# Kernel optimization log

Measured on AMD Instinct MI355X. Metric: run time of the kernel, lower is better.

## Reference

```python
import jax, jax.numpy as jnp
import numpy as np
import math

B_SZ = 2
SEQ = 4000
D_MODEL = 768
D_INNER = 1536
D_STATE = 16
D_CONV = 4
DT_RANK = 48
NSLICES = 5


def setup_inputs() -> dict:
    key = jax.random.key(0)
    ks = jax.random.split(key, 9)
    s = 0.02
    hidden_states = jax.random.normal(ks[0], (B_SZ, SEQ, D_MODEL), jnp.float32)
    in_proj_w = jax.random.normal(ks[1], (2 * D_INNER, D_MODEL), jnp.float32) * s
    conv_w = jax.random.normal(ks[2], (3, D_INNER, 1, D_CONV), jnp.float32) * 0.3
    x_proj_w = jax.random.normal(ks[3], (3, DT_RANK + 2 * D_STATE, D_INNER), jnp.float32) * s
    dt_proj_w = jax.random.uniform(ks[4], (3, D_INNER, DT_RANK), jnp.float32,
                                   -(DT_RANK ** -0.5), DT_RANK ** -0.5)
    # dt bias: inverse-softplus of dt ~ LogUniform(1e-3, 0.1), as in the torch init
    dt = jnp.exp(jax.random.uniform(ks[5], (3, D_INNER), jnp.float32)
                 * (math.log(0.1) - math.log(1e-3)) + math.log(1e-3))
    dt = jnp.clip(dt, 1e-4, None)
    dt_bias = dt + jnp.log(-jnp.expm1(-dt))
    A = jnp.broadcast_to(jnp.arange(1, D_STATE + 1, dtype=jnp.float32), (D_INNER, D_STATE))
    A_log = jnp.broadcast_to(jnp.log(A), (3, D_INNER, D_STATE))
    D_param = jnp.ones((3, D_INNER), jnp.float32)
    out_proj_w = jax.random.normal(ks[6], (D_MODEL, D_INNER), jnp.float32) * s
    return dict(hidden_states=hidden_states, in_proj_w=in_proj_w, conv_w=conv_w,
                x_proj_w=x_proj_w, dt_proj_w=dt_proj_w, dt_bias=dt_bias,
                A_log=A_log, D_param=D_param, out_proj_w=out_proj_w)


def _mamba_branch(xz, cw, xpw, dpw, db, A_log, Dv):
    # xz: [B, 2*d_inner, L]. Equivalent of mamba_inner_fn_no_out_proj.
    x, z = jnp.split(xz, 2, axis=1)                      # [B, d, L] each
    # depthwise causal conv1d (left pad d_conv-1, output length L)
    xc = jax.lax.conv_general_dilated(
        x, cw, window_strides=(1,), padding=[(D_CONV - 1, 0)],
        feature_group_count=D_INNER,
        dimension_numbers=('NCH', 'OIH', 'NCH'))
    x = jax.nn.silu(xc)
    x_dbl = jnp.einsum('bdl,ed->bel', x, xpw)            # [B, dt_rank+2n, L]
    dtr, Bm, Cm = jnp.split(x_dbl, [DT_RANK, DT_RANK + D_STATE], axis=1)
    delta = jax.nn.softplus(jnp.einsum('brl,dr->bdl', dtr, dpw) + db[None, :, None])
    A = -jnp.exp(A_log)                                  # [d, n]

    def step(h, inp):
        d_t, x_t, B_t, C_t = inp                         # [B,d],[B,d],[B,n],[B,n]
        h = h * jnp.exp(d_t[..., None] * A) + (d_t * x_t)[..., None] * B_t[:, None, :]
        y = jnp.einsum('bdn,bn->bd', h, C_t)
        return h, y

    inputs = (jnp.moveaxis(delta, 2, 0), jnp.moveaxis(x, 2, 0),
              jnp.moveaxis(Bm, 2, 0), jnp.moveaxis(Cm, 2, 0))
    h0 = jnp.zeros((x.shape[0], D_INNER, D_STATE), x.dtype)
    _, ys = jax.lax.scan(step, h0, inputs)               # ys: [L, B, d]
    y = jnp.moveaxis(ys, 0, 2)                           # [B, d, L]
    y = y + Dv[None, :, None] * x
    return y * jax.nn.silu(z)


def reference(hidden_states, in_proj_w, conv_w, x_proj_w, dt_proj_w, dt_bias,
              A_log, D_param, out_proj_w):
    b, l, _ = hidden_states.shape
    lc = l // NSLICES
    xz = jnp.einsum('bld,ed->bel', hidden_states, in_proj_w)   # [B, 2d, L]
    # branch 0: forward
    out0 = _mamba_branch(xz, conv_w[0], x_proj_w[0], dt_proj_w[0], dt_bias[0],
                         A_log[0], D_param[0])
    # branch 1: reversed sequence
    out1 = _mamba_branch(xz[:, :, ::-1], conv_w[1], x_proj_w[1], dt_proj_w[1],
                         dt_bias[1], A_log[1], D_param[1])[:, :, ::-1]
    # branch 2: slice-interleaved (chunk into nslices, stack, flatten)
    xz2 = xz.reshape(b, 2 * D_INNER, NSLICES, lc).transpose(0, 1, 3, 2).reshape(b, 2 * D_INNER, l)
    out2 = _mamba_branch(xz2, conv_w[2], x_proj_w[2], dt_proj_w[2], dt_bias[2],
                         A_log[2], D_param[2])
    out2 = out2.reshape(b, D_INNER, lc, NSLICES).transpose(0, 1, 3, 2).reshape(b, D_INNER, l)
    out = out0 + out1 + out2
    return jnp.einsum('bdl,od->blo', out, out_proj_w)          # [B, L, d_model]
```

## Files before the change

kernel.cpp:

```cpp
#include <hip/hip_runtime.h>
#include <math.h>

#define L_SEQ 4000
#define DM 768
#define DI 1536
#define DS 16
#define DTRK 48
#define NCH 50
#define LC 80
#define NBL 8000

typedef __attribute__((ext_vector_type(8))) short short8;
typedef __attribute__((ext_vector_type(8))) unsigned short ushort8;
typedef __attribute__((ext_vector_type(4))) unsigned short ushort4v;
typedef __attribute__((ext_vector_type(4))) float floatx4;
typedef __attribute__((ext_vector_type(2))) float float2v;

__device__ __forceinline__ float silu_f(float x) { return x / (1.f + __expf(-x)); }
__device__ __forceinline__ float softplus_f(float x) {
  return fmaxf(x, 0.f) + __logf(1.f + __expf(-fabsf(x)));
}
__device__ __forceinline__ int map_t(int branch, int t) {
  if (branch == 0) return t;
  if (branch == 1) return L_SEQ - 1 - t;
  return (t % 5) * 800 + t / 5;
}
__device__ __forceinline__ unsigned short f2bf(float f) {
  unsigned int u = __float_as_uint(f);
  u = (u + 0x7fffu + ((u >> 16) & 1u)) >> 16;
  return (unsigned short)u;
}
__device__ __forceinline__ float bf2f(unsigned short u) {
  return __uint_as_float(((unsigned int)u) << 16);
}
__device__ __forceinline__ void glds16(const void* g, void* l) {
  __builtin_amdgcn_global_load_lds((const __attribute__((address_space(1))) void*)g,
                                   (__attribute__((address_space(3))) void*)l, 16, 0, 0);
}
__device__ __forceinline__ void pow_ladder2(float E1, float2v* dc2) {
  float E2 = E1 * E1;
  float E4 = E2 * E2;
  float E8 = E4 * E4;
  float2v v4 = {E4, E4}, v8 = {E8, E8};
  dc2[0] = (float2v){E1, E2};
  dc2[1] = dc2[0] * (float2v){E2, E2};
  dc2[2] = dc2[0] * v4;
  dc2[3] = dc2[1] * v4;
  dc2[4] = dc2[0] * v8;
  dc2[5] = dc2[1] * v8;
  dc2[6] = dc2[2] * v8;
  dc2[7] = dc2[3] * v8;
}

__device__ __forceinline__ void cast_seg(const float* __restrict__ src,
                                         unsigned short* __restrict__ dst,
                                         int blk, int n) {
  int i = (blk * 256 + (int)threadIdx.x) * 8;
  if (i >= n) return;
  float4 v0 = *(const float4*)&src[i];
  float4 v1 = *(const float4*)&src[i + 4];
  ushort8 r;
  r[0] = f2bf(v0.x); r[1] = f2bf(v0.y); r[2] = f2bf(v0.z); r[3] = f2bf(v0.w);
  r[4] = f2bf(v1.x); r[5] = f2bf(v1.y); r[6] = f2bf(v1.z); r[7] = f2bf(v1.w);
  *(ushort8*)&dst[i] = r;
}
__global__ __launch_bounds__(256) void k_cast5(const float* s0, unsigned short* d0,
                                               const float* s1, unsigned short* d1,
                                               const float* s2, unsigned short* d2,
                                               const float* s3, unsigned short* d3,
                                               const float* s4, unsigned short* d4) {
  int blk = blockIdx.x;
  if (blk < 3000)      cast_seg(s0, d0, blk,        6144000);
  else if (blk < 4152) cast_seg(s1, d1, blk - 3000, 2359296);
  else if (blk < 4728) cast_seg(s2, d2, blk - 4152, 1179648);
  else if (blk < 4836) cast_seg(s3, d3, blk - 4728, 221184);
  else                 cast_seg(s4, d4, blk - 4836, 368640);
}

template <int KDIM, int KA, int MODE, int MT, int NBLK, int BMAJ = 0, int NTW = 128>
__global__ __launch_bounds__(256) void k_gemm_bt(const unsigned short* __restrict__ A,
                                                 const unsigned short* __restrict__ B,
                                                 float* __restrict__ O0f,
                                                 unsigned short* __restrict__ O0h,
                                                 unsigned short* __restrict__ O1h) {
  __shared__ unsigned short As[128 * 32];
  __shared__ unsigned short Bs[NTW * 32];
  constexpr int Q = NBLK / 8, R = NBLK % 8;
  constexpr int NFR = NTW / 32;
  int xcd = blockIdx.x & 7;
  int slot = blockIdx.x >> 3;
  int start = xcd * Q + (xcd < R ? xcd : R);
  int j = start + slot;
  int m0 = (j % MT) * 128;
  int n0 = (j / MT) * NTW;
  int tid = threadIdx.x;
  int lane = tid & 63;
  int wm = (tid >> 6) & 1;
  int wn = tid >> 7;
  int srow = tid >> 2;
  int skof = (((tid & 3) ^ ((tid >> 3) & 3)) * 8);
  int brow0 = n0 + srow;       if (brow0 >= NBL) brow0 = NBL - 1;
  int brow1 = n0 + srow + 64;  if (brow1 >= NBL) brow1 = NBL - 1;
  size_t rb0a = 0, rb0b = 0, rb0c = 0, rb1a = 0, rb1b = 0, rb1c = 0;
  if (BMAJ) {
    int bb0 = brow0 >= L_SEQ ? 1 : 0, l0 = brow0 - bb0 * L_SEQ;
    int t1_0 = L_SEQ - 1 - l0;
    int t2_0 = 5 * (l0 % 800) + l0 / 800;
    rb0a = ((size_t)(0 + bb0) * L_SEQ + l0) * DI;
    rb0b = ((size_t)(2 + bb0) * L_SEQ + t1_0) * DI;
    rb0c = ((size_t)(4 + bb0) * L_SEQ + t2_0) * DI;
    if (NTW == 128) {
      int bb1 = brow1 >= L_SEQ ? 1 : 0, l1 = brow1 - bb1 * L_SEQ;
      int t1_1 = L_SEQ - 1 - l1;
      int t2_1 = 5 * (l1 % 800) + l1 / 800;
      rb1a = ((size_t)(0 + bb1) * L_SEQ + l1) * DI;
      rb1b = ((size_t)(2 + bb1) * L_SEQ + t1_1) * DI;
      rb1c = ((size_t)(4 + bb1) * L_SEQ + t2_1) * DI;
    }
  }
  floatx4 zero = {0.f, 0.f, 0.f, 0.f};
  floatx4 acc[4][NFR];
#pragma unroll
  for (int i = 0; i < 4; ++i)
#pragma unroll
    for (int j2 = 0; j2 < NFR; ++j2) acc[i][j2] = zero;
  int ar = wm * 64 + (lane & 15);
  int br = wn * (NTW / 2) + (lane & 15);
  int kq = (((lane >> 4) ^ ((lane >> 1) & 3)) * 8);
  int brnk = 0, dd0 = 0;
  for (int k0 = 0; k0 < KDIM; k0 += 32) {
    int ka = (k0 % KA);
    glds16(&A[(size_t)(m0 + srow) * KA + ka + skof],      &As[tid * 8]);
    glds16(&A[(size_t)(m0 + srow + 64) * KA + ka + skof], &As[tid * 8 + 2048]);
    if (BMAJ) {
      size_t b0 = brnk == 0 ? rb0a : (brnk == 1 ? rb0b : rb0c);
      glds16(&B[b0 + dd0 + skof], &Bs[tid * 8]);
      if (NTW == 128) {
        size_t b1 = brnk == 0 ? rb1a : (brnk == 1 ? rb1b : rb1c);
        glds16(&B[b1 + dd0 + skof], &Bs[tid * 8 + 2048]);
      }
      dd0 += 32;
      if (dd0 == DI) { dd0 = 0; ++brnk; }
    } else {
      glds16(&B[(size_t)brow0 * KDIM + k0 + skof], &Bs[tid * 8]);
      if (NTW == 128)
        glds16(&B[(size_t)brow1 * KDIM + k0 + skof], &Bs[tid * 8 + 2048]);
    }
    __syncthreads();
    short8 a[4], b[NFR];
#pragma unroll
    for (int i = 0; i < 4; ++i) a[i] = *(const short8*)&As[(ar + i * 16) * 32 + kq];
#pragma unroll
    for (int i = 0; i < NFR; ++i) b[i] = *(const short8*)&Bs[(br + i * 16) * 32 + kq];
#pragma unroll
    for (int mt = 0; mt < 4; ++mt)
#pragma unroll
      for (int nt = 0; nt < NFR; ++nt)
        acc[mt][nt] = __builtin_amdgcn_mfma_f32_16x16x32_bf16(a[mt], b[nt], acc[mt][nt], 0, 0, 0);
    __syncthreads();
  }
  int mq = m0 + wm * 64 + ((lane >> 4) << 2);
  int nq = n0 + wn * (NTW / 2) + (lane & 15);
#pragma unroll
  for (int nt = 0; nt < NFR; ++nt) {
    int n = nq + nt * 16;
    if (n >= NBL) continue;
#pragma unroll
    for (int mt = 0; mt < 4; ++mt) {
      int m = mq + mt * 16;
      floatx4 v = acc[mt][nt];
      if (MODE == 0) {
        *(floatx4*)&O0f[(size_t)n * DM + m] = v;
      } else {
        if (m < DI) {
          ushort4v r;
          r[0] = f2bf(v[0]); r[1] = f2bf(v[1]); r[2] = f2bf(v[2]); r[3] = f2bf(v[3]);
          *(ushort4v*)&O0h[(size_t)n * DI + m] = r;
        } else {
          ushort4v r;
          r[0] = f2bf(silu_f(v[0])); r[1] = f2bf(silu_f(v[1]));
          r[2] = f2bf(silu_f(v[2])); r[3] = f2bf(silu_f(v[3]));
          *(ushort4v*)&O1h[(size_t)n * DI + m - DI] = r;
        }
      }
    }
  }
}

__global__ __launch_bounds__(256) void k_conv_all(const unsigned short* __restrict__ xTB,
                                                  const float* __restrict__ cw_all,
                                                  unsigned short* __restrict__ xaB) {
  int z = blockIdx.z;
  int brn = z >> 1, b = z & 1;
  int d = blockIdx.x * 256 + threadIdx.x;
  int t0 = blockIdx.y * 8;
  const unsigned short* xrow = xTB + (size_t)b * L_SEQ * DI;
  float4 w = *(const float4*)&cw_all[((size_t)brn * DI + d) * 4];
  float xm3 = (t0 >= 3) ? bf2f(xrow[(size_t)map_t(brn, t0 - 3) * DI + d]) : 0.f;
  float xm2 = (t0 >= 2) ? bf2f(xrow[(size_t)map_t(brn, t0 - 2) * DI + d]) : 0.f;
  float xm1 = (t0 >= 1) ? bf2f(xrow[(size_t)map_t(brn, t0 - 1) * DI + d]) : 0.f;
#pragma unroll
  for (int i = 0; i < 8; ++i) {
    int t = t0 + i;
    float xc = bf2f(xrow[(size_t)map_t(brn, t) * DI + d]);
    float xa = silu_f(fmaf(w.w, xc, fmaf(w.z, xm1, fmaf(w.y, xm2, w.x * xm3))));
    xaB[((size_t)z * L_SEQ + t) * DI + d] = f2bf(xa);
    xm3 = xm2; xm2 = xm1; xm1 = xc;
  }
}

__global__ __launch_bounds__(256) void k_xprojm(const unsigned short* __restrict__ xpwB,
                                                const unsigned short* __restrict__ xaB,
                                                unsigned short* __restrict__ dtrB,
                                                float* __restrict__ BC) {
  __shared__ unsigned short As[128 * 32];
  __shared__ unsigned short Bs[128 * 32];
  int z = blockIdx.z;
  int brn = z >> 1;
  int n0 = blockIdx.x * 128;
  int tid = threadIdx.x;
  int lane = tid & 63;
  int wm = (tid >> 6) & 1;
  int wn = tid >> 7;
  int srow = tid >> 2;
  int skof = (((tid & 3) ^ ((tid >> 3) & 3)) * 8);
  int arow0 = srow;       if (arow0 > 79) arow0 = 79;
  int arow1 = srow + 64;  if (arow1 > 79) arow1 = 79;
  int brow0 = n0 + srow;       if (brow0 >= L_SEQ) brow0 = L_SEQ - 1;
  int brow1 = n0 + srow + 64;  if (brow1 >= L_SEQ) brow1 = L_SEQ - 1;
  const unsigned short* A = xpwB + (size_t)brn * 80 * DI;
  const unsigned short* Bm = xaB + (size_t)z * L_SEQ * DI;
  floatx4 zero = {0.f, 0.f, 0.f, 0.f};
  floatx4 acc[4][4];
#pragma unroll
  for (int i = 0; i < 4; ++i)
#pragma unroll
    for (int j = 0; j < 4; ++j) acc[i][j] = zero;
  int ar = wm * 64 + (lane & 15);
  int br = wn * 64 + (lane & 15);
  int kq = (((lane >> 4) ^ ((lane >> 1) & 3)) * 8);
  for (int k0 = 0; k0 < DI; k0 += 32) {
    glds16(&A[(size_t)arow0 * DI + k0 + skof], &As[tid * 8]);
    glds16(&A[(size_t)arow1 * DI + k0 + skof], &As[tid * 8 + 2048]);
    glds16(&Bm[(size_t)brow0 * DI + k0 + skof], &Bs[tid * 8]);
    glds16(&Bm[(size_t)brow1 * DI + k0 + skof], &Bs[tid * 8 + 2048]);
    __syncthreads();
    short8 a[4], b[4];
#pragma unroll
    for (int i = 0; i < 4; ++i) a[i] = *(const short8*)&As[(ar + i * 16) * 32 + kq];
#pragma unroll
    for (int i = 0; i < 4; ++i) b[i] = *(const short8*)&Bs[(br + i * 16) * 32 + kq];
#pragma unroll
    for (int mt = 0; mt < 4; ++mt)
#pragma unroll
      for (int nt = 0; nt < 4; ++nt)
        acc[mt][nt] = __builtin_amdgcn_mfma_f32_16x16x32_bf16(a[mt], b[nt], acc[mt][nt], 0, 0, 0);
    __syncthreads();
  }
  int mq = wm * 64 + ((lane >> 4) << 2);
  int nq = n0 + wn * 64 + (lane & 15);
#pragma unroll
  for (int nt = 0; nt < 4; ++nt) {
    int t = nq + nt * 16;
    if (t >= L_SEQ) continue;
#pragma unroll
    for (int mt = 0; mt < 4; ++mt) {
      int j = mq + mt * 16;
      if (j >= 80) continue;
      floatx4 v = acc[mt][nt];
      if (j < 48) {
        ushort4v r;
        r[0] = f2bf(v[0]); r[1] = f2bf(v[1]); r[2] = f2bf(v[2]); r[3] = f2bf(v[3]);
        *(ushort4v*)&dtrB[((size_t)z * L_SEQ + t) * DTRK + j] = r;
      } else {
#pragma unroll
        for (int r = 0; r < 4; ++r)
          BC[((size_t)z * 32 + (j + r - 48)) * L_SEQ + t] = v[r];
      }
    }
  }
}

__global__ __launch_bounds__(256) void k_dtg(const unsigned short* __restrict__ dpwB,
                                             const unsigned short* __restrict__ dtrB,
                                             const float* __restrict__ dbias,
                                             unsigned short* __restrict__ dT) {
  __shared__ unsigned short As[128 * 64];
  __shared__ unsigned short Bs[128 * 64];
  int z = blockIdx.z;
  int brn = z >> 1;
  int m0 = blockIdx.y * 128;
  int n0 = blockIdx.x * 128;
  int tid = threadIdx.x;
  int lane = tid & 63;
  int wm = (tid >> 6) & 1;
  int wn = tid >> 7;
  {
    int zr = tid >> 1, zs = 6 + (tid & 1);
    ushort8 zz = {0, 0, 0, 0, 0, 0, 0, 0};
    *(ushort8*)&As[zr * 64 + ((zs ^ (zr & 7)) << 3)] = zz;
    *(ushort8*)&Bs[zr * 64 + ((zs ^ (zr & 7)) << 3)] = zz;
  }
  {
    int row = tid >> 1;
    int p0 = (tid & 1) * 3;
    const unsigned short* Ag = dpwB + (size_t)brn * DI * DTRK + (size_t)(m0 + row) * DTRK;
    int bro = n0 + row; if (bro > L_SEQ - 1) bro = L_SEQ - 1;
    const unsigned short* Bg = dtrB + ((size_t)z * L_SEQ + bro) * DTRK;
#pragma unroll
    for (int i = 0; i < 3; ++i) {
      int slot = p0 + i;
      int off = (slot ^ (row & 7)) << 3;
      *(ushort8*)&As[row * 64 + off] = *(const ushort8*)&Ag[slot << 3];
      *(ushort8*)&Bs[row * 64 + off] = *(const ushort8*)&Bg[slot << 3];
    }
  }
  __syncthreads();
  int ar = wm * 64 + (lane & 15);
  int brr = wn * 64 + (lane & 15);
  int kslot = lane >> 4;
  floatx4 zero = {0.f, 0.f, 0.f, 0.f};
  floatx4 acc[4][4];
#pragma unroll
  for (int i = 0; i < 4; ++i)
#pragma unroll
    for (int j = 0; j < 4; ++j) acc[i][j] = zero;
#pragma unroll
  for (int kk = 0; kk < 2; ++kk) {
    short8 a[4], b[4];
    int slot = kk * 4 + kslot;
#pragma unroll
    for (int i = 0; i < 4; ++i) {
      int r = ar + i * 16;
      a[i] = *(const short8*)&As[r * 64 + ((slot ^ (r & 7)) << 3)];
    }
#pragma unroll
    for (int i = 0; i < 4; ++i) {
      int r = brr + i * 16;
      b[i] = *(const short8*)&Bs[r * 64 + ((slot ^ (r & 7)) << 3)];
    }
#pragma unroll
    for (int mt = 0; mt < 4; ++mt)
#pragma unroll
      for (int nt = 0; nt < 4; ++nt)
        acc[mt][nt] = __builtin_amdgcn_mfma_f32_16x16x32_bf16(a[mt], b[nt], acc[mt][nt], 0, 0, 0);
  }
  int mq = m0 + wm * 64 + ((lane >> 4) << 2);
  int nq = n0 + wn * 64 + (lane & 15);
  float4 bi[4];
#pragma unroll
  for (int mt = 0; mt < 4; ++mt)
    bi[mt] = *(const float4*)&dbias[(size_t)brn * DI + mq + mt * 16];
#pragma unroll
  for (int nt = 0; nt < 4; ++nt) {
    int n = nq + nt * 16;
    if (n >= L_SEQ) continue;
#pragma unroll
    for (int mt = 0; mt < 4; ++mt) {
      int m = mq + mt * 16;
      floatx4 v = acc[mt][nt];
      ushort4v r;
      r[0] = f2bf(softplus_f(v[0] + bi[mt].x));
      r[1] = f2bf(softplus_f(v[1] + bi[mt].y));
      r[2] = f2bf(softplus_f(v[2] + bi[mt].z));
      r[3] = f2bf(softplus_f(v[3] + bi[mt].w));
      *(ushort4v*)&dT[((size_t)z * L_SEQ + n) * DI + m] = r;
    }
  }
}

__device__ __forceinline__ void load_a2(const float* __restrict__ A_log, int brn, int d,
                                        float* a2, bool& fastp) {
  fastp = true;
#pragma unroll
  for (int g = 0; g < 4; ++g) {
    float4 v = *(const float4*)&A_log[((size_t)brn * DI + d) * DS + g * 4];
    float av0 = __expf(v.x), av1 = __expf(v.y), av2 = __expf(v.z), av3 = __expf(v.w);
    a2[g * 4 + 0] = -av0 * 1.44269504f; a2[g * 4 + 1] = -av1 * 1.44269504f;
    a2[g * 4 + 2] = -av2 * 1.44269504f; a2[g * 4 + 3] = -av3 * 1.44269504f;
    fastp = fastp && fabsf(av0 - (float)(g * 4 + 1)) < 1e-3f
                  && fabsf(av1 - (float)(g * 4 + 2)) < 1e-3f
                  && fabsf(av2 - (float)(g * 4 + 3)) < 1e-3f
                  && fabsf(av3 - (float)(g * 4 + 4)) < 1e-3f;
  }
}

#define S1_BODY(T, XV, DLV)                                                       \
  do {                                                                            \
    S += (DLV);                                                                   \
    float dtx_ = (DLV) * (XV);                                                    \
    float2v dc2[8];                                                               \
    if (fastp) {                                                                  \
      pow_ladder2(exp2f(-(DLV) * 1.44269504f), dc2);                              \
    } else {                                                                      \
      _Pragma("unroll")                                                           \
      for (int i = 0; i < 8; ++i)                                                 \
        dc2[i] = (float2v){exp2f((DLV) * a2[2 * i]), exp2f((DLV) * a2[2 * i + 1])}; \
    }                                                                             \
    const float2v* B2 = (const float2v*)&BtS[(T)][0];                             \
    float2v dtx2 = {dtx_, dtx_};                                                  \
    _Pragma("unroll")                                                             \
    for (int i = 0; i < 8; ++i)                                                   \
      h2[i] = __builtin_elementwise_fma(h2[i], dc2[i], dtx2 * B2[i]);             \
  } while (0)

__global__ __launch_bounds__(256) void k_scan1c(const unsigned short* __restrict__ xaB,
                                                const unsigned short* __restrict__ dT,
                                                const float* __restrict__ BC,
                                                const float* __restrict__ A_log,
                                                float* __restrict__ hO,
                                                float* __restrict__ Sc) {
  __shared__ float BtS[LC][16];
  int z = blockIdx.z;
  int brn = z >> 1;
  int ch = blockIdx.y;
  int t0 = ch * LC;
  int d = blockIdx.x * 256 + threadIdx.x;
  int tid = threadIdx.x;
  for (int i = tid; i < 320; i += 256) {
    int row = i / 20;
    int c4 = (i % 20) * 4;
    float4 v = *(const float4*)&BC[((size_t)z * 32 + row) * L_SEQ + t0 + c4];
    BtS[c4 + 0][row] = v.x; BtS[c4 + 1][row] = v.y;
    BtS[c4 + 2][row] = v.z; BtS[c4 + 3][row] = v.w;
  }
  float a2[16]; bool fastp;
  load_a2(A_log, brn, d, a2, fastp);
  const unsigned short* xbp = xaB + ((size_t)z * L_SEQ + t0) * DI + d;
  const unsigned short* dbp = dT + ((size_t)z * L_SEQ + t0) * DI + d;
  float2v h2[8];
#pragma unroll
  for (int i = 0; i < 8; ++i) h2[i] = (float2v){0.f, 0.f};
  float S = 0.f;
  unsigned short rx_a = xbp[0],      rd_a = dbp[0];
  unsigned short rx_b = xbp[DI],     rd_b = dbp[DI];
  unsigned short rx_c = xbp[2 * DI], rd_c = dbp[2 * DI];
  unsigned short rx_d = xbp[3 * DI], rd_d = dbp[3 * DI];
  __syncthreads();
  for (int t4 = 0; t4 < LC; t4 += 4) {
    { float xv = bf2f(rx_a), dv = bf2f(rd_a); S1_BODY(t4 + 0, xv, dv); }
    { int tc = (t4 + 4 < LC) ? t4 + 4 : LC - 1; rx_a = xbp[tc * DI]; rd_a = dbp[tc * DI]; }
    { float xv = bf2f(rx_b), dv = bf2f(rd_b); S1_BODY(t4 + 1, xv, dv); }
    { int tc = (t4 + 5 < LC) ? t4 + 5 : LC - 1; rx_b = xbp[tc * DI]; rd_b = dbp[tc * DI]; }
    { float xv = bf2f(rx_c), dv = bf2f(rd_c); S1_BODY(t4 + 2, xv, dv); }
    { int tc = (t4 + 6 < LC) ? t4 + 6 : LC - 1; rx_c = xbp[tc * DI]; rd_c = dbp[tc * DI]; }
    { float xv = bf2f(rx_d), dv = bf2f(rd_d); S1_BODY(t4 + 3, xv, dv); }
    { int tc = (t4 + 7 < LC) ? t4 + 7 : LC - 1; rx_d = xbp[tc * DI]; rd_d = dbp[tc * DI]; }
  }
  size_t base = (((size_t)z * NCH + ch) * DI + d) * 16;
#pragma unroll
  for (int i = 0; i < 8; ++i) *(float2v*)&hO[base + i * 2] = h2[i];
  Sc[((size_t)z * NCH + ch) * DI + d] = S;
}

__global__ __launch_bounds__(256) void k_scan2c(float* __restrict__ hO,
                                                const float* __restrict__ Sc,
                                                const float* __restrict__ A_log) {
  int idx = blockIdx.x * 256 + threadIdx.x;
  int z = idx / (DI * 16);
  int rem = idx % (DI * 16);
  int brn = z >> 1;
  float a2 = -__expf(A_log[(size_t)brn * DI * DS + rem]) * 1.44269504f;
  const int HS = DI * 16;
  size_t p = (size_t)z * NCH * HS + rem;
  size_t q = (size_t)z * NCH * DI + (rem >> 4);
  float th_a = hO[p];            float s_a = Sc[q];
  float th_b = hO[p + HS];       float s_b = Sc[q + DI];
  float th_c = hO[p + 2 * HS];   float s_c = Sc[q + 2 * DI];
  float th_d = hO[p + 3 * HS];   float s_d = Sc[q + 3 * DI];
  float H = 0.f;
  for (int c4 = 0; c4 < 48; c4 += 4) {
    hO[p] = H; H = fmaf(exp2f(s_a * a2), H, th_a);
    th_a = hO[p + 4 * HS]; s_a = Sc[q + 4 * DI];
    p += HS; q += DI;
    hO[p] = H; H = fmaf(exp2f(s_b * a2), H, th_b);
    th_b = hO[p + 4 * HS]; s_b = Sc[q + 4 * DI];
    p += HS; q += DI;
    hO[p] = H; H = fmaf(exp2f(s_c * a2), H, th_c);
    if (c4 + 6 < NCH) { th_c = hO[p + 4 * HS]; s_c = Sc[q + 4 * DI]; }
    p += HS; q += DI;
    hO[p] = H; H = fmaf(exp2f(s_d * a2), H, th_d);
    if (c4 + 7 < NCH) { th_d = hO[p + 4 * HS]; s_d = Sc[q + 4 * DI]; }
    p += HS; q += DI;
  }
  hO[p] = H; H = fmaf(exp2f(s_a * a2), H, th_a); p += HS;
  hO[p] = H;
}

#define S3D(T, XV, DLV, SZV)                                                      \
  do {                                                                            \
    float dtx_ = (DLV) * (XV);                                                    \
    float2v dc2[8];                                                               \
    if (fastp) {                                                                  \
      pow_ladder2(exp2f(-(DLV) * 1.44269504f), dc2);                              \
    } else {                                                                      \
      _Pragma("unroll")                                                           \
      for (int i = 0; i < 8; ++i)                                                 \
        dc2[i] = (float2v){exp2f((DLV) * a2[2 * i]), exp2f((DLV) * a2[2 * i + 1])}; \
    }                                                                             \
    const float2v* B2 = (const float2v*)&BCt[(T)][0];                             \
    const float2v* C2 = (const float2v*)&BCt[(T)][16];                            \
    float2v dtx2 = {dtx_, dtx_};                                                  \
    float2v y2a = {0.f, 0.f}, y2b = {0.f, 0.f};                                   \
    _Pragma("unroll")                                                             \
    for (int i = 0; i < 4; ++i) {                                                 \
      h2[i] = __builtin_elementwise_fma(h2[i], dc2[i], dtx2 * B2[i]);             \
      y2a = __builtin_elementwise_fma(h2[i], C2[i], y2a);                         \
    }                                                                             \
    _Pragma("unroll")                                                             \
    for (int i = 4; i < 8; ++i) {                                                 \
      h2[i] = __builtin_elementwise_fma(h2[i], dc2[i], dtx2 * B2[i]);             \
      y2b = __builtin_elementwise_fma(h2[i], C2[i], y2b);                         \
    }                                                                             \
    float y_ = (y2a[0] + y2a[1]) + (y2b[0] + y2b[1]) + Dv * (XV);                 \
    dp[(size_t)(T) * DI] = f2bf(y_ * (SZV));                                      \
  } while (0)

__global__ __launch_bounds__(256) void k_scan3d(const unsigned short* __restrict__ xaB,
                                                unsigned short* __restrict__ dT,
                                                const float* __restrict__ BC,
                                                const float* __restrict__ A_log,
                                                const float* __restrict__ Dp,
                                                const float* __restrict__ hO,
                                                const unsigned short* __restrict__ szTB) {
  __shared__ float BCt[LC][32];
  int z = blockIdx.z;
  int brn = z >> 1, b = z & 1;
  int ch = blockIdx.y;
  int t0 = ch * LC;
  int d = blockIdx.x * 256 + threadIdx.x;
  int tid = threadIdx.x;
  for (int i = tid; i < 640; i += 256) {
    int row = i / 20;
    int c4 = (i % 20) * 4;
    float4 v = *(const float4*)&BC[((size_t)z * 32 + row) * L_SEQ + t0 + c4];
    BCt[c4 + 0][row] = v.x; BCt[c4 + 1][row] = v.y;
    BCt[c4 + 2][row] = v.z; BCt[c4 + 3][row] = v.w;
  }
  float a2[16]; bool fastp;
  load_a2(A_log, brn, d, a2, fastp);
  float Dv = Dp[(size_t)brn * DI + d];
  const unsigned short* xp = xaB + ((size_t)z * L_SEQ + t0) * DI + d;
  unsigned short* dp = dT + ((size_t)z * L_SEQ + t0) * DI + d;
  const unsigned short* szb = szTB + (size_t)b * L_SEQ * DI + d;
  float2v h2[8];
  size_t hbase = (((size_t)z * NCH + ch) * DI + d) * 16;
#pragma unroll
  for (int i = 0; i < 8; ++i) h2[i] = *(const float2v*)&hO[hbase + i * 2];
  bool isb2 = (brn == 2);
  int mbase = (brn == 1) ? (L_SEQ - 1 - t0) : t0;
  int msign = (brn == 1) ? -1 : 1;
  int chb = ch * 16;
  auto mrow = [&](int tt) -> int {
    if (isb2) return (tt % 5) * 800 + chb + tt / 5;
    return mbase + msign * tt;
  };
  unsigned short rx_a = xp[0],      rl_a = dp[0],      rs_a = szb[(size_t)mrow(0) * DI];
  unsigned short rx_b = xp[DI],     rl_b = dp[DI],     rs_b = szb[(size_t)mrow(1) * DI];
  unsigned short rx_c = xp[2 * DI], rl_c = dp[2 * DI], rs_c = szb[(size_t)mrow(2) * DI];
  unsigned short rx_d = xp[3 * DI], rl_d = dp[3 * DI], rs_d = szb[(size_t)mrow(3) * DI];
  __syncthreads();
  for (int t4 = 0; t4 < LC; t4 += 4) {
    { float xv = bf2f(rx_a), dv = bf2f(rl_a), sv = bf2f(rs_a); S3D(t4 + 0, xv, dv, sv); }
    { int tc = (t4 + 4 < LC) ? t4 + 4 : LC - 1;
      rx_a = xp[(size_t)tc * DI]; rl_a = dp[(size_t)tc * DI]; rs_a = szb[(size_t)mrow(tc) * DI]; }
    { float xv = bf2f(rx_b), dv = bf2f(rl_b), sv = bf2f(rs_b); S3D(t4 + 1, xv, dv, sv); }
    { int tc = (t4 + 5 < LC) ? t4 + 5 : LC - 1;
      rx_b = xp[(size_t)tc * DI]; rl_b = dp[(size_t)tc * DI]; rs_b = szb[(size_t)mrow(tc) * DI]; }
    { float xv = bf2f(rx_c), dv = bf2f(rl_c), sv = bf2f(rs_c); S3D(t4 + 2, xv, dv, sv); }
    { int tc = (t4 + 6 < LC) ? t4 + 6 : LC - 1;
      rx_c = xp[(size_t)tc * DI]; rl_c = dp[(size_t)tc * DI]; rs_c = szb[(size_t)mrow(tc) * DI]; }
    { float xv = bf2f(rx_d), dv = bf2f(rl_d), sv = bf2f(rs_d); S3D(t4 + 3, xv, dv, sv); }
    { int tc = (t4 + 7 < LC) ? t4 + 7 : LC - 1;
      rx_d = xp[(size_t)tc * DI]; rl_d = dp[(size_t)tc * DI]; rs_d = szb[(size_t)mrow(tc) * DI]; }
  }
}

extern "C" void kernel_launch(void* const* d_in, const int* in_sizes, int n_in,
                              void* d_out, int out_size, void* d_ws, size_t ws_size,
                              hipStream_t stream) {
  const float* hs        = (const float*)d_in[0];
  const float* in_proj_w = (const float*)d_in[1];
  const float* conv_w    = (const float*)d_in[2];
  const float* x_proj_w  = (const float*)d_in[3];
  const float* dt_proj_w = (const float*)d_in[4];
  const float* dt_bias   = (const float*)d_in[5];
  const float* A_log     = (const float*)d_in[6];
  const float* D_param   = (const float*)d_in[7];
  const float* out_proj_w= (const float*)d_in[8];
  float* out = (float*)d_out;
  float* ws = (float*)d_ws;

  unsigned short* xTB  = (unsigned short*)(ws);
  unsigned short* szTB = (unsigned short*)(ws + 6144000);
  unsigned short* dtrB = (unsigned short*)(ws + 12288000);
  float* BC            = ws + 12864000;
  unsigned short* dT   = (unsigned short*)(ws + 13632000);
  float* hO            = ws + 32064000;
  float* Sc            = ws + 39436800;
  unsigned short* dpwB = (unsigned short*)(ws + 39897600);
  unsigned short* OWb  = (unsigned short*)(ws + 40008192);
  unsigned short* hsB  = (unsigned short*)(ws + 40598016);
  unsigned short* Wb   = hsB + 6144000;
  unsigned short* xaB  = (unsigned short*)(ws + 40598016);
  unsigned short* xpwB = (unsigned short*)(ws + 59030016);

  k_cast5<<<5016, 256, 0, stream>>>(hs, hsB, in_proj_w, Wb, out_proj_w, OWb,
                                    dt_proj_w, dpwB, x_proj_w, xpwB);

  k_gemm_bt<DM, DM, 1, 24, 1512><<<1512, 256, 0, stream>>>(Wb, hsB, nullptr, xTB, szTB);

  k_conv_all<<<dim3(6, 500, 6), 256, 0, stream>>>(xTB, conv_w, xaB);
  k_xprojm<<<dim3(32, 1, 6), 256, 0, stream>>>(xpwB, xaB, dtrB, BC);
  k_dtg<<<dim3(32, 12, 6), 256, 0, stream>>>(dpwB, dtrB, dt_bias, dT);

  k_scan1c<<<dim3(6, NCH, 6), 256, 0, stream>>>(xaB, dT, BC, A_log, hO, Sc);
  k_scan2c<<<576, 256, 0, stream>>>(hO, Sc, A_log);
  k_scan3d<<<dim3(6, NCH, 6), 256, 0, stream>>>(xaB, dT, BC, A_log, D_param, hO, szTB);

  k_gemm_bt<3 * DI, DI, 0, 6, 750, 1, 64><<<750, 256, 0, stream>>>(OWb, dT, out, nullptr, nullptr);
}
```

Before: 532.6 us.

## Double-buffer LDS tiles in bf16 MFMA GEMM to overlap loads with compute

Allocates two LDS buffers for the A and B tiles and issues the global-to-LDS loads for the next K step before computing on the current one, leaving one barrier per iteration. This is meant to hide global memory latency behind the MFMA work. LDS use per block doubles, which may lower occupancy. The loop relies on a single barrier to order the async glds writes against the next iteration's reads, which could be a correctness risk if those loads are not waited on.

```diff
diff --git a/kernel.cpp b/kernel.cpp
--- a/kernel.cpp
+++ b/kernel.cpp
@@ -83,8 +83,8 @@
                                                  float* __restrict__ O0f,
                                                  unsigned short* __restrict__ O0h,
                                                  unsigned short* __restrict__ O1h) {
-  __shared__ unsigned short As[128 * 32];
-  __shared__ unsigned short Bs[NTW * 32];
+  __shared__ unsigned short As[2][128 * 32];
+  __shared__ unsigned short Bs[2][NTW * 32];
   constexpr int Q = NBLK / 8, R = NBLK % 8;
   constexpr int NFR = NTW / 32;
   int xcd = blockIdx.x & 7;
@@ -118,6 +118,25 @@
       rb1c = ((size_t)(4 + bb1) * L_SEQ + t2_1) * DI;
     }
   }
+  auto stage = [&](int buf, int k0) {
+    int ka = (k0 % KA);
+    glds16(&A[(size_t)(m0 + srow) * KA + ka + skof],      &As[buf][tid * 8]);
+    glds16(&A[(size_t)(m0 + srow + 64) * KA + ka + skof], &As[buf][tid * 8 + 2048]);
+    if (BMAJ) {
+      int brnk = k0 / DI;
+      int dd0 = k0 - brnk * DI;
+      size_t b0 = brnk == 0 ? rb0a : (brnk == 1 ? rb0b : rb0c);
+      glds16(&B[b0 + dd0 + skof], &Bs[buf][tid * 8]);
+      if (NTW == 128) {
+        size_t b1 = brnk == 0 ? rb1a : (brnk == 1 ? rb1b : rb1c);
+        glds16(&B[b1 + dd0 + skof], &Bs[buf][tid * 8 + 2048]);
+      }
+    } else {
+      glds16(&B[(size_t)brow0 * KDIM + k0 + skof], &Bs[buf][tid * 8]);
+      if (NTW == 128)
+        glds16(&B[(size_t)brow1 * KDIM + k0 + skof], &Bs[buf][tid * 8 + 2048]);
+    }
+  };
   floatx4 zero = {0.f, 0.f, 0.f, 0.f};
   floatx4 acc[4][NFR];
 #pragma unroll
@@ -127,37 +146,23 @@
   int ar = wm * 64 + (lane & 15);
   int br = wn * (NTW / 2) + (lane & 15);
   int kq = (((lane >> 4) ^ ((lane >> 1) & 3)) * 8);
-  int brnk = 0, dd0 = 0;
+  stage(0, 0);
+  __syncthreads();
+  int cur = 0;
   for (int k0 = 0; k0 < KDIM; k0 += 32) {
-    int ka = (k0 % KA);
-    glds16(&A[(size_t)(m0 + srow) * KA + ka + skof],      &As[tid * 8]);
-    glds16(&A[(size_t)(m0 + srow + 64) * KA + ka + skof], &As[tid * 8 + 2048]);
-    if (BMAJ) {
-      size_t b0 = brnk == 0 ? rb0a : (brnk == 1 ? rb0b : rb0c);
-      glds16(&B[b0 + dd0 + skof], &Bs[tid * 8]);
-      if (NTW == 128) {
-        size_t b1 = brnk == 0 ? rb1a : (brnk == 1 ? rb1b : rb1c);
-        glds16(&B[b1 + dd0 + skof], &Bs[tid * 8 + 2048]);
-      }
-      dd0 += 32;
-      if (dd0 == DI) { dd0 = 0; ++brnk; }
-    } else {
-      glds16(&B[(size_t)brow0 * KDIM + k0 + skof], &Bs[tid * 8]);
-      if (NTW == 128)
-        glds16(&B[(size_t)brow1 * KDIM + k0 + skof], &Bs[tid * 8 + 2048]);
-    }
-    __syncthreads();
+    if (k0 + 32 < KDIM) stage(cur ^ 1, k0 + 32);
     short8 a[4], b[NFR];
 #pragma unroll
-    for (int i = 0; i < 4; ++i) a[i] = *(const short8*)&As[(ar + i * 16) * 32 + kq];
-#pragma unroll
-    for (int i = 0; i < NFR; ++i) b[i] = *(const short8*)&Bs[(br + i * 16) * 32 + kq];
+    for (int i = 0; i < 4; ++i) a[i] = *(const short8*)&As[cur][(ar + i * 16) * 32 + kq];
+#pragma unroll
+    for (int i = 0; i < NFR; ++i) b[i] = *(const short8*)&Bs[cur][(br + i * 16) * 32 + kq];
 #pragma unroll
     for (int mt = 0; mt < 4; ++mt)
 #pragma unroll
       for (int nt = 0; nt < NFR; ++nt)
         acc[mt][nt] = __builtin_amdgcn_mfma_f32_16x16x32_bf16(a[mt], b[nt], acc[mt][nt], 0, 0, 0);
     __syncthreads();
+    cur ^= 1;
   }
   int mq = m0 + wm * 64 + ((lane >> 4) << 2);
   int nq = n0 + wn * (NTW / 2) + (lane & 15);
```

Result: slower. 682.1 us (+28.1%).
